# Kernel tuning notes

Measured on AMD Instinct MI355X. Metric: run time of the kernel, lower is better.

The kernel has to match this reference:

```python
import jax, jax.numpy as jnp
import numpy as np

# graph layout constants
B = 64        # number of graphs
NPG = 512     # nodes per graph
N = B * NPG   # total nodes
DEG = 16      # avg degree
E = N * DEG   # total edges
F_IN = 256
H, C = 4, 64  # heads, per-head dim
K = NPG // 2  # topk pooling keeps ratio=0.5 per graph


def setup_inputs() -> dict:
    key = jax.random.key(0)
    ks = jax.random.split(key, 8)
    x = jax.random.normal(ks[0], (N, F_IN), dtype=jnp.float32)
    # within-graph random edges (src -> dst), contiguous node ids per graph
    offs = jnp.repeat(jnp.arange(B, dtype=jnp.int64) * NPG, NPG * DEG)
    src = offs + jax.random.randint(ks[1], (E,), 0, NPG)
    dst = offs + jax.random.randint(ks[2], (E,), 0, NPG)
    edge_index = jnp.stack([src, dst]).astype(jnp.int64)
    W = jax.random.normal(ks[3], (F_IN, H, C), dtype=jnp.float32) / np.sqrt(F_IN)
    att_src = jax.random.normal(ks[4], (H, C), dtype=jnp.float32) / np.sqrt(C)
    att_dst = jax.random.normal(ks[5], (H, C), dtype=jnp.float32) / np.sqrt(C)
    bias = jnp.zeros((H * C,), dtype=jnp.float32)
    bn_gamma = jnp.ones((H * C,), dtype=jnp.float32)
    bn_beta = jnp.zeros((H * C,), dtype=jnp.float32)
    pool_weight = jax.random.normal(ks[6], (H * C,), dtype=jnp.float32) / np.sqrt(H * C)
    return {"x": x, "edge_index": edge_index, "W": W, "att_src": att_src,
            "att_dst": att_dst, "bias": bias, "bn_gamma": bn_gamma,
            "bn_beta": bn_beta, "pool_weight": pool_weight}


def reference(x, edge_index, W, att_src, att_dst, bias, bn_gamma, bn_beta, pool_weight):
    n = x.shape[0]
    # --- GATConv ---
    h = jnp.einsum('nf,fhc->nhc', x, W)                 # [N,H,C]
    a_src = jnp.sum(h * att_src, axis=-1)               # [N,H]
    a_dst = jnp.sum(h * att_dst, axis=-1)               # [N,H]
    loops = jnp.arange(n, dtype=edge_index.dtype)        # add_self_loops=True default
    src = jnp.concatenate([edge_index[0], loops])
    dst = jnp.concatenate([edge_index[1], loops])
    e = jax.nn.leaky_relu(a_src[src] + a_dst[dst], 0.2)  # [E+N,H]
    # scatter-softmax over edges grouped by destination node
    emax = jax.ops.segment_max(e, dst, num_segments=n)
    ex = jnp.exp(e - emax[dst])
    den = jax.ops.segment_sum(ex, dst, num_segments=n)
    alpha = ex / (den[dst] + 1e-16)                      # [E+N,H]
    msg = alpha[:, :, None] * h[src]                     # [E+N,H,C]
    out = jax.ops.segment_sum(msg, dst, num_segments=n)  # [N,H,C]
    feat = out.reshape(n, H * C) + bias                  # concat heads
    # --- ReLU + BatchNorm (batch stats, training mode) ---
    feat = jax.nn.relu(feat)
    mean = jnp.mean(feat, axis=0)
    var = jnp.var(feat, axis=0)
    feat = (feat - mean) * jax.lax.rsqrt(var + 1e-5) * bn_gamma + bn_beta
    # --- TopKPooling (score = x.w/||w||, keep top ratio per graph, gate by tanh) ---
    score = feat @ pool_weight / jnp.linalg.norm(pool_weight)  # [N]
    top_s, top_i = jax.lax.top_k(score.reshape(B, NPG), K)     # [B,K]
    fg = feat.reshape(B, NPG, H * C)
    sel = jnp.take_along_axis(fg, top_i[:, :, None], axis=1)    # [B,K,HC]
    pooled = sel * jnp.tanh(top_s)[:, :, None]
    return pooled.reshape(B * K, H * C)
```

## Files before the change

kernel.cpp:

```cpp
#include <hip/hip_runtime.h>
#include <math.h>

#define N_NODES 32768
#define NPG 512
#define NGRAPH 64
#define KKEEP 256
#define CAP 64

typedef __attribute__((ext_vector_type(8))) short short8;
typedef __attribute__((ext_vector_type(4))) float f32x4;

__device__ __forceinline__ unsigned short f2bf(float v) {
  unsigned u = __builtin_bit_cast(unsigned, v);
  u = (u + 0x7FFFu + ((u >> 16) & 1u)) >> 16;
  return (unsigned short)u;
}
__device__ __forceinline__ float bf2f(unsigned short u) {
  unsigned v = ((unsigned)u) << 16;
  return __builtin_bit_cast(float, v);
}

__device__ __forceinline__ void async_cp16(unsigned short* l, const unsigned short* g) {
  __builtin_amdgcn_global_load_lds(
      (const __attribute__((address_space(1))) unsigned int*)g,
      (__attribute__((address_space(3))) unsigned int*)l, 16, 0, 0);
}

__device__ __forceinline__ void block_barrier() {
  __builtin_amdgcn_sched_barrier(0);
  asm volatile("s_barrier" ::: "memory");
  __builtin_amdgcn_sched_barrier(0);
}
__device__ __forceinline__ void wait_all() {
  asm volatile("s_waitcnt vmcnt(0) lgkmcnt(0)" ::: "memory");
  __builtin_amdgcn_sched_barrier(0);
}

__global__ __launch_bounds__(256) void k_conv(
    const float* __restrict__ W,
    unsigned short* __restrict__ wth, unsigned short* __restrict__ wtl,
    unsigned short* __restrict__ wtll, int* __restrict__ cnt) {
  const int t = threadIdx.x;
  if (blockIdx.x >= 64) {
    int i = (blockIdx.x - 64) * 1024 + t * 4;
    *(int4*)&cnt[i] = make_int4(0, 0, 0, 0);
    return;
  }
  int n = blockIdx.x * 4 + (t >> 6);
  int k = (t & 63) * 4;
  unsigned short hb[4], lb[4], qb[4];
#pragma unroll
  for (int j = 0; j < 4; j++) {
    float v = W[(size_t)(k + j) * 256 + n];
    unsigned short hh = f2bf(v);
    float e1 = v - bf2f(hh);
    unsigned short ll = f2bf(e1);
    float e2 = e1 - bf2f(ll);
    hb[j] = hh; lb[j] = ll; qb[j] = f2bf(e2);
  }
  *(uint2*)&wth[(size_t)n * 256 + k] = *(uint2*)&hb[0];
  *(uint2*)&wtl[(size_t)n * 256 + k] = *(uint2*)&lb[0];
  *(uint2*)&wtll[(size_t)n * 256 + k] = *(uint2*)&qb[0];
}

#define A_STR 129
#define A_SZ 12384
#define B_BASE 12384
#define B_SZ 12288
__global__ __launch_bounds__(512, 4) void k_gemm_hist(
    const float* __restrict__ x,
    const unsigned short* __restrict__ wth, const unsigned short* __restrict__ wtl,
    const unsigned short* __restrict__ wtll,
    const float* __restrict__ attS, const float* __restrict__ attD,
    float* __restrict__ h, float* __restrict__ a_src, float* __restrict__ a_dst,
    const int* __restrict__ ei, int E, int* __restrict__ cnt,
    unsigned short* __restrict__ nbr) {
  __shared__ unsigned short lds[36960];
  const int t = threadIdx.x;
  const int bid = blockIdx.x;
  if (bid >= 512) {
    int e = (bid - 512) * 512 + t;
    if (e < E) {
      int s = ei[e];
      int d = ei[E + e];
      int slot = atomicAdd(&cnt[d], 1);
      if (slot < CAP) nbr[(size_t)d * CAP + slot] = (unsigned short)(s & (NPG - 1));
    }
    return;
  }
  const int mb = (bid & 7) * 32 + (bid >> 4);
  const int nh = (bid >> 3) & 1;
  const int row0 = mb * 128;
  const int wid = t >> 6, lane = t & 63;
  const int q = lane >> 4, ln = lane & 15;
  const int wm = (wid >> 1) * 32, wn = (wid & 1) * 64;
  const int sr = t >> 2, scq = t & 3;
  f32x4 acc[2][4] = {};

  {
    size_t ga = (size_t)(row0 + sr) * 256 + scq * 8;
    float4 f0 = *(const float4*)&x[ga];
    float4 f1 = *(const float4*)&x[ga + 4];
    float ff[8] = {f0.x, f0.y, f0.z, f0.w, f1.x, f1.y, f1.z, f1.w};
    unsigned short hs[8], ls[8], qs[8];
#pragma unroll
    for (int j = 0; j < 8; j++) {
      unsigned short hh = f2bf(ff[j]);
      float e1 = ff[j] - bf2f(hh);
      unsigned short ll = f2bf(e1);
      float e2 = e1 - bf2f(ll);
      hs[j] = hh; ls[j] = ll; qs[j] = f2bf(e2);
    }
    *(uint4*)&lds[((0 * 4 + scq) * A_STR + sr) * 8] = *(uint4*)&hs[0];
    *(uint4*)&lds[((1 * 4 + scq) * A_STR + sr) * 8] = *(uint4*)&ls[0];
    *(uint4*)&lds[((2 * 4 + scq) * A_STR + sr) * 8] = *(uint4*)&qs[0];
    size_t gb = (size_t)(nh * 128 + (t & 127)) * 256 + (t >> 7) * 8;
    async_cp16(&lds[B_BASE + 0 * 4096 + t * 8], &wth[gb]);
    async_cp16(&lds[B_BASE + 1 * 4096 + t * 8], &wtl[gb]);
    async_cp16(&lds[B_BASE + 2 * 4096 + t * 8], &wtll[gb]);
  }
  wait_all();
  block_barrier();

  for (int kc = 0; kc < 8; kc++) {
    const int cur = kc & 1;
    float4 f0, f1;
    if (kc < 7) {
      const int k1 = (kc + 1) * 32;
      size_t ga = (size_t)(row0 + sr) * 256 + k1 + scq * 8;
      f0 = *(const float4*)&x[ga];
      f1 = *(const float4*)&x[ga + 4];
      unsigned short* bb = &lds[B_BASE + (cur ^ 1) * B_SZ];
      size_t gb = (size_t)(nh * 128 + (t & 127)) * 256 + k1 + (t >> 7) * 8;
      async_cp16(&bb[0 * 4096 + t * 8], &wth[gb]);
      async_cp16(&bb[1 * 4096 + t * 8], &wtl[gb]);
      async_cp16(&bb[2 * 4096 + t * 8], &wtll[gb]);
    }
    const unsigned short* bc = &lds[B_BASE + cur * B_SZ];
    short8 ah[2], al[2], aq[2];
#pragma unroll
    for (int mt = 0; mt < 2; mt++) {
      int r = wm + mt * 16 + ln;
      ah[mt] = *(const short8*)&lds[((0 * 4 + q) * A_STR + r) * 8];
      al[mt] = *(const short8*)&lds[((1 * 4 + q) * A_STR + r) * 8];
      aq[mt] = *(const short8*)&lds[((2 * 4 + q) * A_STR + r) * 8];
    }
#pragma unroll
    for (int nt = 0; nt < 4; nt++) {
      int r = wn + nt * 16 + ln;
      short8 bh = *(const short8*)&bc[0 * 4096 + (q * 128 + r) * 8];
      short8 bl = *(const short8*)&bc[1 * 4096 + (q * 128 + r) * 8];
      short8 bq = *(const short8*)&bc[2 * 4096 + (q * 128 + r) * 8];
#pragma unroll
      for (int mt = 0; mt < 2; mt++) {
        acc[mt][nt] = __builtin_amdgcn_mfma_f32_16x16x32_bf16(ah[mt], bh, acc[mt][nt], 0, 0, 0);
        acc[mt][nt] = __builtin_amdgcn_mfma_f32_16x16x32_bf16(ah[mt], bl, acc[mt][nt], 0, 0, 0);
        acc[mt][nt] = __builtin_amdgcn_mfma_f32_16x16x32_bf16(al[mt], bh, acc[mt][nt], 0, 0, 0);
        acc[mt][nt] = __builtin_amdgcn_mfma_f32_16x16x32_bf16(ah[mt], bq, acc[mt][nt], 0, 0, 0);
        acc[mt][nt] = __builtin_amdgcn_mfma_f32_16x16x32_bf16(al[mt], bl, acc[mt][nt], 0, 0, 0);
        acc[mt][nt] = __builtin_amdgcn_mfma_f32_16x16x32_bf16(aq[mt], bh, acc[mt][nt], 0, 0, 0);
      }
    }
    unsigned short hs[8], ls[8], qs[8];
    if (kc < 7) {
      float ff[8] = {f0.x, f0.y, f0.z, f0.w, f1.x, f1.y, f1.z, f1.w};
#pragma unroll
      for (int j = 0; j < 8; j++) {
        unsigned short hh = f2bf(ff[j]);
        float e1 = ff[j] - bf2f(hh);
        unsigned short ll = f2bf(e1);
        float e2 = e1 - bf2f(ll);
        hs[j] = hh; ls[j] = ll; qs[j] = f2bf(e2);
      }
    }
    block_barrier();
    if (kc < 7) {
      *(uint4*)&lds[((0 * 4 + scq) * A_STR + sr) * 8] = *(uint4*)&hs[0];
      *(uint4*)&lds[((1 * 4 + scq) * A_STR + sr) * 8] = *(uint4*)&ls[0];
      *(uint4*)&lds[((2 * 4 + scq) * A_STR + sr) * 8] = *(uint4*)&qs[0];
    }
    wait_all();
    block_barrier();
  }

  const int head = nh * 2 + (wid & 1);
  float sA[4], sD[4];
#pragma unroll
  for (int nt = 0; nt < 4; nt++) {
    int n = nh * 128 + wn + nt * 16 + ln;
    sA[nt] = attS[n];
    sD[nt] = attD[n];
  }
  float2* epi = (float2*)lds;
#pragma unroll
  for (int mt = 0; mt < 2; mt++) {
#pragma unroll
    for (int reg = 0; reg < 4; reg++) {
      int m = row0 + wm + mt * 16 + q * 4 + reg;
      float ps = 0.f, pd = 0.f;
#pragma unroll
      for (int nt = 0; nt < 4; nt++) {
        float v = acc[mt][nt][reg];
        h[(size_t)m * 256 + nh * 128 + wn + nt * 16 + ln] = v;
        ps = fmaf(v, sA[nt], ps);
        pd = fmaf(v, sD[nt], pd);
      }
      epi[(((wid * 4 + q) * 8) + mt * 4 + reg) * 18 + (ln ^ (q * 4))] =
          make_float2(ps, pd);
    }
  }
  __syncthreads();
  if (lane < 32) {
    const int rr2 = lane & 7;
    const int q2 = lane >> 3;
    const int base = (((wid * 4 + q2) * 8) + rr2) * 18;
    float ps = 0.f, pd = 0.f;
#pragma unroll
    for (int i = 0; i < 16; i++) {
      float2 v = epi[base + (i ^ (q2 * 4))];
      ps += v.x;
      pd += v.y;
    }
    int m = row0 + wm + (rr2 >> 2) * 16 + q2 * 4 + (rr2 & 3);
    a_src[m * 4 + head] = ps;
    a_dst[m * 4 + head] = pd;
  }
}

__global__ __launch_bounds__(256) void k_agg(
    const float* __restrict__ h, const float* __restrict__ a_src,
    const float* __restrict__ a_dst, const int* __restrict__ cnt,
    const unsigned short* __restrict__ nbr, const float* __restrict__ bias,
    float* __restrict__ feat) {
  __shared__ float p_lds[4][68][4];
  __shared__ int s_lds[4][68];
  const int wv = threadIdx.x >> 6;
  const int lane = threadIdx.x & 63;
  int nb = (blockIdx.x & 7) * (N_NODES / 4 / 8) + (blockIdx.x >> 3);
  const int node = nb * 4 + wv;
  const int head = lane >> 4;
  const int li = lane & 15;
  const int c0 = lane * 4;
  const int base = node & ~(NPG - 1);
  const float ad = a_dst[node * 4 + head];
  int n = cnt[node];
  if (n > CAP) n = CAP;
  float e_reg[5];
  int srcs[5];
  int nit = 0;
  float m = -1e30f;
  for (int j = li; j <= n; j += 16) {
    int s = (j < n) ? base + (int)nbr[(size_t)node * CAP + j] : node;
    float e = a_src[s * 4 + head] + ad;
    e = (e > 0.f) ? e : 0.2f * e;
    srcs[nit] = s;
    e_reg[nit++] = e;
    m = fmaxf(m, e);
  }
#pragma unroll
  for (int d = 1; d < 16; d <<= 1) m = fmaxf(m, __shfl_xor(m, d, 16));
  float l = 0.f;
  for (int i = 0; i < nit; i++) {
    int j = li + i * 16;
    float p = __expf(e_reg[i] - m);
    l += p;
    p_lds[wv][j][head] = p;
    if (head == 0) s_lds[wv][j] = srcs[i];
  }
#pragma unroll
  for (int d = 1; d < 16; d <<= 1) l += __shfl_xor(l, d, 16);
  const float linv = 1.f / (l + 1e-16f);
  __builtin_amdgcn_s_waitcnt(0);
  float4 acc0 = make_float4(0.f, 0.f, 0.f, 0.f);
  float4 acc1 = make_float4(0.f, 0.f, 0.f, 0.f);
  int j = 0;
  for (; j + 1 <= n; j += 2) {
    float p0 = p_lds[wv][j][head];
    float p1 = p_lds[wv][j + 1][head];
    int s0 = s_lds[wv][j];
    int s1 = s_lds[wv][j + 1];
    float4 h0 = *(const float4*)&h[(size_t)s0 * 256 + c0];
    float4 h1 = *(const float4*)&h[(size_t)s1 * 256 + c0];
    acc0.x = fmaf(p0, h0.x, acc0.x); acc1.x = fmaf(p1, h1.x, acc1.x);
    acc0.y = fmaf(p0, h0.y, acc0.y); acc1.y = fmaf(p1, h1.y, acc1.y);
    acc0.z = fmaf(p0, h0.z, acc0.z); acc1.z = fmaf(p1, h1.z, acc1.z);
    acc0.w = fmaf(p0, h0.w, acc0.w); acc1.w = fmaf(p1, h1.w, acc1.w);
  }
  if (j <= n) {
    float p0 = p_lds[wv][j][head];
    int s0 = s_lds[wv][j];
    float4 h0 = *(const float4*)&h[(size_t)s0 * 256 + c0];
    acc0.x = fmaf(p0, h0.x, acc0.x);
    acc0.y = fmaf(p0, h0.y, acc0.y);
    acc0.z = fmaf(p0, h0.z, acc0.z);
    acc0.w = fmaf(p0, h0.w, acc0.w);
  }
  const float4 b4 = *(const float4*)&bias[c0];
  float4 o;
  o.x = fmaxf(fmaf(acc0.x + acc1.x, linv, b4.x), 0.f);
  o.y = fmaxf(fmaf(acc0.y + acc1.y, linv, b4.y), 0.f);
  o.z = fmaxf(fmaf(acc0.z + acc1.z, linv, b4.z), 0.f);
  o.w = fmaxf(fmaf(acc0.w + acc1.w, linv, b4.w), 0.f);
  *(float4*)&feat[(size_t)node * 256 + c0] = o;
}

__global__ __launch_bounds__(64) void k_bn_partial(const float* __restrict__ feat,
                                                   double* __restrict__ psum,
                                                   double* __restrict__ psq) {
  const int chunk = blockIdx.x >> 2;
  const int c = (blockIdx.x & 3) * 64 + threadIdx.x;
  const int r0 = chunk * 128;
  double s = 0.0, q = 0.0;
  for (int i = 0; i < 128; i++) {
    double v = (double)feat[(size_t)(r0 + i) * 256 + c];
    s += v;
    q += v * v;
  }
  psum[chunk * 256 + c] = s;
  psq[chunk * 256 + c] = q;
}

__global__ __launch_bounds__(1024) void k_bn_final(
    const double* __restrict__ psum, const double* __restrict__ psq,
    const float* __restrict__ gam, const float* __restrict__ bet,
    const float* __restrict__ pw, float* __restrict__ cA, float* __restrict__ cB,
    float* __restrict__ sv) {
  __shared__ double reds[4][256];
  __shared__ double redq[4][256];
  __shared__ double wsq[256];
  __shared__ double sb[256];
  const int t = threadIdx.x;
  const int c = t & 255, sl = t >> 8;
  double s = 0.0, q = 0.0;
  for (int i = sl * 64; i < sl * 64 + 64; i++) {
    s += psum[i * 256 + c];
    q += psq[i * 256 + c];
  }
  reds[sl][c] = s;
  redq[sl][c] = q;
  if (sl == 0) {
    double w = (double)pw[c];
    wsq[c] = w * w;
  }
  __syncthreads();
  if (t == 0) {
    double nn = 0.0;
    for (int i = 0; i < 256; i++) nn += wsq[i];
    wsq[0] = sqrt(nn);
  }
  __syncthreads();
  if (sl == 0) {
    s = reds[0][c] + reds[1][c] + reds[2][c] + reds[3][c];
    q = redq[0][c] + redq[1][c] + redq[2][c] + redq[3][c];
    double mean = s / (double)N_NODES;
    double var = q / (double)N_NODES - mean * mean;
    double a = (double)gam[c] / sqrt(var + 1e-5);
    double cb = (double)bet[c] - mean * a;
    cA[c] = (float)a;
    cB[c] = (float)cb;
    double pwnv = (double)pw[c] / wsq[0];
    sv[c] = (float)(a * pwnv);
    sb[c] = cb * pwnv;
  }
  __syncthreads();
  if (t == 0) {
    double s0 = 0.0;
    for (int i = 0; i < 256; i++) s0 += sb[i];
    sv[256] = (float)s0;
  }
}

__global__ __launch_bounds__(256) void k_score(
    const float* __restrict__ feat, const float* __restrict__ sv,
    float* __restrict__ score) {
  const int lane = threadIdx.x & 63;
  const int node = blockIdx.x * 4 + (threadIdx.x >> 6);
  const int c0 = lane * 4;
  float4 f = *(const float4*)&feat[(size_t)node * 256 + c0];
  float4 w = *(const float4*)&sv[c0];
  float p = f.x * w.x + f.y * w.y + f.z * w.z + f.w * w.w;
#pragma unroll
  for (int d = 1; d < 64; d <<= 1) p += __shfl_xor(p, d, 64);
  if (lane == 0) score[node] = p + sv[256];
}

__global__ __launch_bounds__(256) void k_topk(
    const float* __restrict__ score, const float* __restrict__ feat,
    const float* __restrict__ cA, const float* __restrict__ cB,
    float* __restrict__ out) {
  __shared__ float ss[NPG];
  __shared__ int rnk[64];
  __shared__ float gt[64];
  const int g = blockIdx.x >> 3;
  const int part = blockIdx.x & 7;
  const int t = threadIdx.x;
  ss[t] = score[g * NPG + t];
  ss[t + 256] = score[g * NPG + t + 256];
  __syncthreads();
  const int ln = t & 3;
  const int ndl = part * 64 + (t >> 2);
  const float s = ss[ndl];
  int rank = 0;
  for (int j = ln * 128; j < ln * 128 + 128; j++) {
    float sj = ss[j];
    rank += (sj > s || (sj == s && j < ndl)) ? 1 : 0;
  }
  rank += __shfl_xor(rank, 1);
  rank += __shfl_xor(rank, 2);
  if (ln == 0) {
    rnk[t >> 2] = rank;
    gt[t >> 2] = tanhf(s);
  }
  __syncthreads();
  for (int idx = t; idx < 64 * 64; idx += 256) {
    int r = idx >> 6;
    int rank2 = rnk[r];
    if (rank2 < KKEEP) {
      int c4 = (idx & 63) * 4;
      int node = g * NPG + part * 64 + r;
      float4 f = *(const float4*)&feat[(size_t)node * 256 + c4];
      float4 a = *(const float4*)&cA[c4];
      float4 b = *(const float4*)&cB[c4];
      float tg = gt[r];
      float4 o;
      o.x = fmaf(f.x, a.x, b.x) * tg;
      o.y = fmaf(f.y, a.y, b.y) * tg;
      o.z = fmaf(f.z, a.z, b.z) * tg;
      o.w = fmaf(f.w, a.w, b.w) * tg;
      *(float4*)&out[(size_t)(g * KKEEP + rank2) * 256 + c4] = o;
    }
  }
}

extern "C" void kernel_launch(void* const* d_in, const int* in_sizes, int n_in,
                              void* d_out, int out_size, void* d_ws, size_t ws_size,
                              hipStream_t stream) {
  const float* x    = (const float*)d_in[0];
  const int*   ei   = (const int*)d_in[1];
  const float* W    = (const float*)d_in[2];
  const float* attS = (const float*)d_in[3];
  const float* attD = (const float*)d_in[4];
  const float* bias = (const float*)d_in[5];
  const float* gam  = (const float*)d_in[6];
  const float* bet  = (const float*)d_in[7];
  const float* pw   = (const float*)d_in[8];
  float* out = (float*)d_out;
  const int E = in_sizes[1] / 2;

  char* p = (char*)d_ws;
  float* h     = (float*)p; p += (size_t)N_NODES * 256 * 4;
  float* feat  = (float*)p; p += (size_t)N_NODES * 256 * 4;
  float* a_src = (float*)p; p += (size_t)N_NODES * 4 * 4;
  float* a_dst = (float*)p; p += (size_t)N_NODES * 4 * 4;
  float* score = (float*)p; p += (size_t)N_NODES * 4;
  double* psum = (double*)p; p += (size_t)256 * 256 * 8;
  double* psq  = (double*)p; p += (size_t)256 * 256 * 8;
  float* cA    = (float*)p; p += 256 * 4;
  float* cB    = (float*)p; p += 256 * 4;
  float* sv    = (float*)p; p += 260 * 4;
  unsigned short* wth  = (unsigned short*)p; p += (size_t)256 * 256 * 2;
  unsigned short* wtl  = (unsigned short*)p; p += (size_t)256 * 256 * 2;
  unsigned short* wtll = (unsigned short*)p; p += (size_t)256 * 256 * 2;
  int* cnt     = (int*)p;   p += (size_t)N_NODES * 4;
  unsigned short* nbr = (unsigned short*)p; p += (size_t)N_NODES * CAP * 2;

  k_conv<<<96, 256, 0, stream>>>(W, wth, wtl, wtll, cnt);
  k_gemm_hist<<<1536, 512, 0, stream>>>(x, wth, wtl, wtll, attS, attD,
                                        h, a_src, a_dst, ei, E, cnt, nbr);
  k_agg<<<N_NODES / 4, 256, 0, stream>>>(h, a_src, a_dst, cnt, nbr, bias, feat);
  k_bn_partial<<<1024, 64, 0, stream>>>(feat, psum, psq);
  k_bn_final<<<1, 1024, 0, stream>>>(psum, psq, gam, bet, pw, cA, cB, sv);
  k_score<<<N_NODES / 4, 256, 0, stream>>>(feat, sv, score);
  k_topk<<<NGRAPH * 8, 256, 0, stream>>>(score, feat, cA, cB, out);
}
```

Measured before the change: 204.3 us.

## Fuse BatchNorm statistics into aggregation kernel via last-block atomic counters

Merges the BN partial-sum and final-reduction kernels into the aggregation kernel. Per-chunk atomic counters let the last block to finish a 128-node chunk compute that chunk's column sums, and a global counter lets the last chunk finisher compute the BN coefficients and score vector. This removes two kernel launches and their gaps, at the cost of fences and atomics in every block plus serialized tail work done by a single block. The counters are zeroed in the conversion kernel through one extra block.

```diff
diff --git a/kernel.cpp b/kernel.cpp
--- a/kernel.cpp
+++ b/kernel.cpp
@@ -39,8 +39,14 @@
 __global__ __launch_bounds__(256) void k_conv(
     const float* __restrict__ W,
     unsigned short* __restrict__ wth, unsigned short* __restrict__ wtl,
-    unsigned short* __restrict__ wtll, int* __restrict__ cnt) {
+    unsigned short* __restrict__ wtll, int* __restrict__ cnt,
+    int* __restrict__ chunk_cnt, int* __restrict__ gcnt) {
   const int t = threadIdx.x;
+  if (blockIdx.x >= 96) {
+    chunk_cnt[t] = 0;
+    if (t == 0) gcnt[0] = 0;
+    return;
+  }
   if (blockIdx.x >= 64) {
     int i = (blockIdx.x - 64) * 1024 + t * 4;
     *(int4*)&cnt[i] = make_int4(0, 0, 0, 0);
@@ -64,7 +70,6 @@
 }
 
 #define A_STR 129
-#define A_SZ 12384
 #define B_BASE 12384
 #define B_SZ 12288
 __global__ __launch_bounds__(512, 4) void k_gemm_hist(
@@ -227,13 +232,19 @@
   }
 }
 
-__global__ __launch_bounds__(256) void k_agg(
+__global__ __launch_bounds__(256) void k_agg_bn(
     const float* __restrict__ h, const float* __restrict__ a_src,
     const float* __restrict__ a_dst, const int* __restrict__ cnt,
     const unsigned short* __restrict__ nbr, const float* __restrict__ bias,
-    float* __restrict__ feat) {
+    float* __restrict__ feat, double* __restrict__ psum, double* __restrict__ psq,
+    const float* __restrict__ gam, const float* __restrict__ bet,
+    const float* __restrict__ pw, float* __restrict__ cA, float* __restrict__ cB,
+    float* __restrict__ sv, int* __restrict__ chunk_cnt, int* __restrict__ gcnt) {
   __shared__ float p_lds[4][68][4];
   __shared__ int s_lds[4][68];
+  __shared__ int lastc, lastg;
+  __shared__ double wsqs[256];
+  __shared__ double sbs[256];
   const int wv = threadIdx.x >> 6;
   const int lane = threadIdx.x & 63;
   int nb = (blockIdx.x & 7) * (N_NODES / 4 / 8) + (blockIdx.x >> 3);
@@ -302,71 +313,74 @@
   o.z = fmaxf(fmaf(acc0.z + acc1.z, linv, b4.z), 0.f);
   o.w = fmaxf(fmaf(acc0.w + acc1.w, linv, b4.w), 0.f);
   *(float4*)&feat[(size_t)node * 256 + c0] = o;
-}
-
-__global__ __launch_bounds__(64) void k_bn_partial(const float* __restrict__ feat,
-                                                   double* __restrict__ psum,
-                                                   double* __restrict__ psq) {
-  const int chunk = blockIdx.x >> 2;
-  const int c = (blockIdx.x & 3) * 64 + threadIdx.x;
-  const int r0 = chunk * 128;
-  double s = 0.0, q = 0.0;
-  for (int i = 0; i < 128; i++) {
-    double v = (double)feat[(size_t)(r0 + i) * 256 + c];
-    s += v;
-    q += v * v;
-  }
-  psum[chunk * 256 + c] = s;
-  psq[chunk * 256 + c] = q;
-}
-
-__global__ __launch_bounds__(1024) void k_bn_final(
-    const double* __restrict__ psum, const double* __restrict__ psq,
-    const float* __restrict__ gam, const float* __restrict__ bet,
-    const float* __restrict__ pw, float* __restrict__ cA, float* __restrict__ cB,
-    float* __restrict__ sv) {
-  __shared__ double reds[4][256];
-  __shared__ double redq[4][256];
-  __shared__ double wsq[256];
-  __shared__ double sb[256];
-  const int t = threadIdx.x;
-  const int c = t & 255, sl = t >> 8;
-  double s = 0.0, q = 0.0;
-  for (int i = sl * 64; i < sl * 64 + 64; i++) {
-    s += psum[i * 256 + c];
-    q += psq[i * 256 + c];
-  }
-  reds[sl][c] = s;
-  redq[sl][c] = q;
-  if (sl == 0) {
-    double w = (double)pw[c];
-    wsq[c] = w * w;
-  }
-  __syncthreads();
-  if (t == 0) {
-    double nn = 0.0;
-    for (int i = 0; i < 256; i++) nn += wsq[i];
-    wsq[0] = sqrt(nn);
-  }
-  __syncthreads();
-  if (sl == 0) {
-    s = reds[0][c] + reds[1][c] + reds[2][c] + reds[3][c];
-    q = redq[0][c] + redq[1][c] + redq[2][c] + redq[3][c];
+
+  const int chunk = nb >> 5;
+  __syncthreads();
+  if (threadIdx.x == 0) {
+    __threadfence();
+    lastc = (atomicAdd(&chunk_cnt[chunk], 1) == 31) ? 1 : 0;
+  }
+  __syncthreads();
+  if (!lastc) return;
+  __threadfence();
+  {
+    const int c = threadIdx.x;
+    const int r0 = chunk * 128;
+    double s = 0.0, q = 0.0;
+    for (int i = 0; i < 128; i++) {
+      double v = (double)feat[(size_t)(r0 + i) * 256 + c];
+      s += v;
+      q += v * v;
+    }
+    psum[chunk * 256 + c] = s;
+    psq[chunk * 256 + c] = q;
+  }
+  __syncthreads();
+  if (threadIdx.x == 0) {
+    __threadfence();
+    lastg = (atomicAdd(gcnt, 1) == 255) ? 1 : 0;
+  }
+  __syncthreads();
+  if (!lastg) return;
+  __threadfence();
+  {
+    const int c = threadIdx.x;
+    wsqs[c] = (double)pw[c] * (double)pw[c];
+    __syncthreads();
+    if (threadIdx.x == 0) {
+      double nn = 0.0;
+      for (int i = 0; i < 256; i++) nn += wsqs[i];
+      wsqs[0] = sqrt(nn);
+    }
+    __syncthreads();
+    double gs[4], gq[4];
+#pragma unroll
+    for (int sl = 0; sl < 4; sl++) {
+      double ts = 0.0, tq = 0.0;
+      for (int i = sl * 64; i < sl * 64 + 64; i++) {
+        ts += psum[i * 256 + c];
+        tq += psq[i * 256 + c];
+      }
+      gs[sl] = ts;
+      gq[sl] = tq;
+    }
+    double s = gs[0] + gs[1] + gs[2] + gs[3];
+    double q = gq[0] + gq[1] + gq[2] + gq[3];
     double mean = s / (double)N_NODES;
     double var = q / (double)N_NODES - mean * mean;
     double a = (double)gam[c] / sqrt(var + 1e-5);
     double cb = (double)bet[c] - mean * a;
     cA[c] = (float)a;
     cB[c] = (float)cb;
-    double pwnv = (double)pw[c] / wsq[0];
+    double pwnv = (double)pw[c] / wsqs[0];
     sv[c] = (float)(a * pwnv);
-    sb[c] = cb * pwnv;
-  }
-  __syncthreads();
-  if (t == 0) {
-    double s0 = 0.0;
-    for (int i = 0; i < 256; i++) s0 += sb[i];
-    sv[256] = (float)s0;
+    sbs[c] = cb * pwnv;
+    __syncthreads();
+    if (threadIdx.x == 0) {
+      double s0 = 0.0;
+      for (int i = 0; i < 256; i++) s0 += sbs[i];
+      sv[256] = (float)s0;
+    }
   }
 }
 
@@ -463,13 +477,15 @@
   unsigned short* wtll = (unsigned short*)p; p += (size_t)256 * 256 * 2;
   int* cnt     = (int*)p;   p += (size_t)N_NODES * 4;
   unsigned short* nbr = (unsigned short*)p; p += (size_t)N_NODES * CAP * 2;
-
-  k_conv<<<96, 256, 0, stream>>>(W, wth, wtl, wtll, cnt);
+  int* chunk_cnt = (int*)p; p += 256 * 4;
+  int* gcnt    = (int*)p;   p += 16;
+
+  k_conv<<<97, 256, 0, stream>>>(W, wth, wtl, wtll, cnt, chunk_cnt, gcnt);
   k_gemm_hist<<<1536, 512, 0, stream>>>(x, wth, wtl, wtll, attS, attD,
                                         h, a_src, a_dst, ei, E, cnt, nbr);
-  k_agg<<<N_NODES / 4, 256, 0, stream>>>(h, a_src, a_dst, cnt, nbr, bias, feat);
-  k_bn_partial<<<1024, 64, 0, stream>>>(feat, psum, psq);
-  k_bn_final<<<1, 1024, 0, stream>>>(psum, psq, gam, bet, pw, cA, cB, sv);
+  k_agg_bn<<<N_NODES / 4, 256, 0, stream>>>(h, a_src, a_dst, cnt, nbr, bias,
+                                            feat, psum, psq, gam, bet, pw,
+                                            cA, cB, sv, chunk_cnt, gcnt);
   k_score<<<N_NODES / 4, 256, 0, stream>>>(feat, sv, score);
   k_topk<<<NGRAPH * 8, 256, 0, stream>>>(score, feat, cA, cB, out);
 }
```

Result: slower. 482.5 us (+136.1%).
